# Performance work log

Measured on AMD Instinct MI355X. Metric: run time of the kernel, lower is better.

The kernel has to match this reference:

```python
import jax, jax.numpy as jnp
import numpy as np

SCALE_BASE = 512.0
GAMMA = 0.96875


def _rotate_every_two(x):
    x1 = x[..., ::2]
    x2 = x[..., 1::2]
    return jnp.stack([-x2, x1], axis=-1).reshape(x.shape)


def _dup_interleave(m):
    # [L, d/2] -> [L, d], each column duplicated: (a,b) -> (a,a,b,b)
    return jnp.repeat(m, 2, axis=-1)


def _xpos(x, downscale=False):
    # x: [B, L, d]; offset = 0 (parallel form)
    B, L, d = x.shape
    half = d // 2
    pos = jnp.arange(L, dtype=x.dtype)
    # xpos per-channel scale base
    sv = (jnp.arange(0, d, 2, dtype=x.dtype) + 0.4 * d) / (1.4 * d)   # [d/2]
    scale = sv[None, :] ** (pos[:, None] / SCALE_BASE)                 # [L, d/2]
    if downscale:
        scale = 1.0 / scale
    inv_freq = 1.0 / (10000.0 ** (jnp.arange(half, dtype=x.dtype) / half))
    sinusoid = pos[:, None] * inv_freq[None, :]                        # [L, d/2]
    sin = _dup_interleave(jnp.sin(sinusoid) * scale)                   # [L, d]
    cos = _dup_interleave(jnp.cos(sinusoid) * scale)                   # [L, d]
    return x * cos[None] + _rotate_every_two(x) * sin[None]


def _get_D(seq_len, dtype):
    idx = jnp.arange(seq_len)
    diff = idx[:, None] - idx[None, :]                                 # n - m
    safe = jnp.where(diff >= 0, diff, 0).astype(dtype)
    return jnp.where(diff >= 0, GAMMA ** safe, jnp.zeros((), dtype))   # [L, L]


def setup_inputs() -> dict:
    key = jax.random.key(0)
    k1, k2, k3, k4 = jax.random.split(key, 4)
    B, L, H, D = 2, 4096, 1024, 64
    X = jax.random.normal(k1, (B, L, H), dtype=jnp.float32)
    W_Q = jax.random.normal(k2, (H, D), dtype=jnp.float32) / H
    W_K = jax.random.normal(k3, (H, D), dtype=jnp.float32) / H
    W_V = jax.random.normal(k4, (H, D), dtype=jnp.float32) / H
    return {"X": X, "W_Q": W_Q, "W_K": W_K, "W_V": W_V}


def reference(X, W_Q, W_K, W_V):
    L = X.shape[1]
    Dmask = _get_D(L, X.dtype)                     # [L, L]
    Q = _xpos(X @ W_Q)                             # [B, L, d]
    K = _xpos(X @ W_K, downscale=True)             # [B, L, d]
    V = X @ W_V                                    # [B, L, v]
    ret = jnp.einsum('bnd,bmd->bnm', Q, K) * Dmask[None]  # [B, L, L]
    return ret @ V                                 # [B, L, v]
```

## Files before the change

### kernel.cpp

```cpp
#include <hip/hip_runtime.h>
#include <math.h>

#define NB 2
#define LL 4096
#define HH 1024
#define DD 64
#define CHK 64
#define NCH 64
#define BLROWS (NB*LL)
#define NCHT (NB*NCH)
#define GAMMA 0.96875f

typedef _Float16 f16x8 __attribute__((ext_vector_type(8)));
typedef _Float16 f16x4 __attribute__((ext_vector_type(4)));
typedef float    f32x4 __attribute__((ext_vector_type(4)));

#define WCH 12288
#define SBS 584

__global__ __launch_bounds__(256) void prep_w(
    const float* __restrict__ WQ, const float* __restrict__ WK,
    const float* __restrict__ WV, _Float16* __restrict__ Whg,
    _Float16* __restrict__ Wlg)
{
    const unsigned t = blockIdx.x * 256 + threadIdx.x;
    const unsigned kchunk = t / 1536u;
    const unsigned s = t - kchunk * 1536u;
    const int ct2  = s >> 6;
    const int lane = s & 63;
    const int n16  = ct2 >> 1;
    const int kt   = ct2 & 1;
    const int quad = lane >> 4;
    const int n    = n16 * 16 + (lane & 15);
    const int k0   = (int)kchunk * 64 + kt * 32 + quad * 8;
    const int m    = n >> 6;
    const int d    = n & 63;
    const float* Wm = (m == 0) ? WQ : (m == 1) ? WK : WV;
    f16x8 hv, lv;
#pragma unroll
    for (int j = 0; j < 8; ++j) {
        const float x = Wm[(size_t)(k0 + j) * DD + d] * 1024.f;
        const _Float16 h = (_Float16)x;
        hv[j] = h;
        lv[j] = (_Float16)(x - (float)h);
    }
    *(f16x8*)&Whg[(size_t)t * 8] = hv;
    *(f16x8*)&Wlg[(size_t)t * 8] = lv;
}

__global__ __launch_bounds__(256) void proj_mfma(
    const float* __restrict__ X, const _Float16* __restrict__ Whg,
    const _Float16* __restrict__ Wlg, _Float16* __restrict__ Qr,
    _Float16* __restrict__ Kf, _Float16* __restrict__ Vf)
{
    __shared__ __align__(16) _Float16 lds[12288];
    _Float16* Xh = lds;
    _Float16* Xl = lds + 2048;
    _Float16* Wh = lds + 4096;
    _Float16* Wl = lds + 8192;

    const int tid  = threadIdx.x;
    const int wv   = tid >> 6;
    const int lane = tid & 63;
    const int quad = lane >> 4;
    const int l15  = lane & 15;
    const int r0   = (blockIdx.x & 255) * 32;
    const int cb4  = (blockIdx.x >> 8) * 4;
    const int rt   = wv & 1;
    const int cp   = (wv >> 1) * 2;

    const int xrow = tid >> 3;
    const int xk8  = (tid & 7) * 8;
    const int xslot = (((xrow >> 4) * 2 + (xk8 >> 5)) * 64 +
                       ((xk8 >> 3) & 3) * 16 + (xrow & 15)) * 8;

    f32x4 acc[2];
    acc[0] = (f32x4){0.f, 0.f, 0.f, 0.f};
    acc[1] = (f32x4){0.f, 0.f, 0.f, 0.f};

    float4 pxa, pxb;
    f16x8  pwh[2], pwl2[2];
    {
        const float* xp = &X[(size_t)(r0 + xrow) * HH + xk8];
        pxa = *(const float4*)&xp[0];
        pxb = *(const float4*)&xp[4];
#pragma unroll
        for (int i = 0; i < 2; ++i) {
            const int s = tid + i * 256;
            const int ctl = s >> 7, kt = (s >> 6) & 1, ln = s & 63;
            const size_t off = (size_t)(((cb4 + ctl) * 2 + kt) * 64 + ln) * 8;
            pwh[i]  = *(const f16x8*)&Whg[off];
            pwl2[i] = *(const f16x8*)&Wlg[off];
        }
    }

    for (int ch = 0; ch < 16; ++ch) {
        __syncthreads();
        {
            const float xv[8] = {pxa.x, pxa.y, pxa.z, pxa.w,
                                 pxb.x, pxb.y, pxb.z, pxb.w};
            f16x8 hv, lv;
#pragma unroll
            for (int e = 0; e < 8; ++e) {
                const _Float16 h = (_Float16)xv[e];
                hv[e] = h;
                lv[e] = (_Float16)(xv[e] - (float)h);
            }
            *(f16x8*)&Xh[xslot] = hv;
            *(f16x8*)&Xl[xslot] = lv;
#pragma unroll
            for (int i = 0; i < 2; ++i) {
                *(f16x8*)&Wh[(tid + i * 256) * 8] = pwh[i];
                *(f16x8*)&Wl[(tid + i * 256) * 8] = pwl2[i];
            }
        }
        __syncthreads();
        if (ch + 1 < 16) {
            const float* xp = &X[(size_t)(r0 + xrow) * HH + (ch + 1) * 64 + xk8];
            pxa = *(const float4*)&xp[0];
            pxb = *(const float4*)&xp[4];
            const size_t cb = (size_t)(ch + 1) * WCH;
#pragma unroll
            for (int i = 0; i < 2; ++i) {
                const int s = tid + i * 256;
                const int ctl = s >> 7, kt = (s >> 6) & 1, ln = s & 63;
                const size_t off = cb +
                    (size_t)(((cb4 + ctl) * 2 + kt) * 64 + ln) * 8;
                pwh[i]  = *(const f16x8*)&Whg[off];
                pwl2[i] = *(const f16x8*)&Wlg[off];
            }
        }
#pragma unroll
        for (int kt = 0; kt < 2; ++kt) {
            const f16x8 aH = *(const f16x8*)&Xh[((rt * 2 + kt) * 64 + lane) * 8];
            const f16x8 aL = *(const f16x8*)&Xl[((rt * 2 + kt) * 64 + lane) * 8];
#pragma unroll
            for (int cj = 0; cj < 2; ++cj) {
                const int ctl = cp + cj;
                const f16x8 bh = *(const f16x8*)&Wh[((ctl * 2 + kt) * 64 + lane) * 8];
                const f16x8 bl = *(const f16x8*)&Wl[((ctl * 2 + kt) * 64 + lane) * 8];
                acc[cj] = __builtin_amdgcn_mfma_f32_16x16x32_f16(aH, bh, acc[cj], 0, 0, 0);
                acc[cj] = __builtin_amdgcn_mfma_f32_16x16x32_f16(aH, bl, acc[cj], 0, 0, 0);
                acc[cj] = __builtin_amdgcn_mfma_f32_16x16x32_f16(aL, bh, acc[cj], 0, 0, 0);
            }
        }
    }

#pragma unroll
    for (int cj = 0; cj < 2; ++cj) {
        const int ctg = cb4 + cp + cj;
        const f32x4 v = acc[cj];
        const int col = ctg * 16 + l15;
        const int mat = ctg >> 2;
        const int d   = col & 63;
        if (mat < 2) {
            const int i2 = d >> 1;
            const float sv   = (2.f * (float)i2 + 25.6f) / 89.6f;
            const float l2sv = log2f(sv);
            const float ifr  = exp2f(-13.28771237954945f * ((float)i2 / 32.f));
            const float sgn  = (mat == 0) ? 1.f : -1.f;
#pragma unroll
            for (int r = 0; r < 4; ++r) {
                const int row = r0 + rt * 16 + quad * 4 + r;
                const float val = v[r] * (1.f / 1024.f);
                const float p = __shfl_xor(val, 1, 64);
                const float pf  = (float)(row & (LL - 1));
                const float pfs = (float)(row & 63);
                const float scl = exp2f(sgn * (pfs * (1.f / 512.f)) * l2sv);
                float s, c;
                sincosf(pf * ifr, &s, &c);
                s *= scl; c *= scl;
                const float o = ((col & 1) == 0) ? val * c - p * s
                                                 : val * c + p * s;
                if (mat == 0) {
                    Qr[(size_t)row * DD + d] = (_Float16)o;
                } else {
                    const int b = row >> 12, posb = row & 4095;
                    Kf[(((size_t)b * 8 + (d >> 3)) * 4096 + posb) * 8 + (d & 7)] =
                        (_Float16)o;
                }
            }
        } else {
            f16x4 vv;
#pragma unroll
            for (int r = 0; r < 4; ++r) vv[r] = (_Float16)(v[r] * (1.f / 1024.f));
            const int row0 = r0 + rt * 16 + quad * 4;
            const int b = row0 >> 12, posb = row0 & 4095;
            *(f16x4*)&Vf[(((size_t)b * 512 + (posb >> 3)) * 64 + d) * 8 + (posb & 7)] = vv;
        }
    }
}

__global__ __launch_bounds__(256) void chunk_out(
    const _Float16* __restrict__ Qr, const _Float16* __restrict__ Kf,
    const _Float16* __restrict__ Vf, float* __restrict__ out)
{
    __shared__ __align__(16) unsigned char smraw[20032];
    _Float16* Sb  = (_Float16*)smraw;
    _Float16* svp = (_Float16*)(smraw + 18688);
    float*    pwl = (float*)(smraw + 19712);

    const int tid   = threadIdx.x;
    const int bc    = blockIdx.x;
    const int chunk = bc >> 2;
    const int qt    = bc & 3;
    const int w     = tid >> 6;
    const int lane  = tid & 63;
    const int quad  = lane >> 4;
    const int l15   = lane & 15;
    const int cloc  = chunk & 63;
    const int bB    = chunk >> 6;
    const size_t rowbase = (size_t)chunk * CHK + qt * 16;
    const float l2g = log2f(GAMMA);

    if (tid < 65) pwl[tid] = exp2f((float)tid * l2g);
#pragma unroll
    for (int e = 0; e < 2; ++e) {
        const int idx = tid + e * 256;
        const int dl  = (idx >> 6) + 1;
        const int dd  = idx & 63;
        const float sv = (2.f * (float)(dd >> 1) + 25.6f) / 89.6f;
        svp[idx] = (_Float16)exp2f(0.125f * (float)dl * log2f(sv));
    }

    f16x8 aQ[2];
#pragma unroll
    for (int ks = 0; ks < 2; ++ks)
        aQ[ks] = *(const f16x8*)&Qr[(rowbase + l15) * DD + ks * 32 + quad * 8];
    __syncthreads();

    {
        const int posb = cloc * 64 + w * 16 + l15;
        f32x4 sA = (f32x4){0.f, 0.f, 0.f, 0.f};
#pragma unroll
        for (int ks = 0; ks < 2; ++ks) {
            const f16x8 bK = *(const f16x8*)&Kf[(((size_t)bB * 8 + ks * 4 + quad)
                                                * 4096 + posb) * 8];
            sA = __builtin_amdgcn_mfma_f32_16x16x32_f16(aQ[ks], bK, sA, 0, 0, 0);
        }
        const int m = w * 16 + l15;
#pragma unroll
        for (int r = 0; r < 4; ++r) {
            const int nl = quad * 4 + r;
            const int n64 = qt * 16 + nl;
            const float val = (n64 >= m) ? sA[r] * pwl[n64 - m] : 0.f;
            Sb[nl * SBS + m] = (_Float16)val;
        }
    }

    for (int jc = w; jc < 32; jc += 4) {
        const int dlt = 8 - (jc >> 2);
        const bool valid = (dlt <= cloc);
        const int mq = (jc * 16 + l15) & 63;
        const float gl = valid ? exp2f((float)(64 * dlt - mq) * l2g) : 0.f;
        const _Float16 glh = (_Float16)gl;
        const int cs = valid ? (chunk - dlt) : chunk;
        const int posb = (cs & 63) * 64 + mq;
        f32x4 sc4 = (f32x4){0.f, 0.f, 0.f, 0.f};
#pragma unroll
        for (int ks = 0; ks < 2; ++ks) {
            const f16x8 bk = *(const f16x8*)&Kf[(((size_t)bB * 8 + ks * 4 + quad)
                                                * 4096 + posb) * 8];
            const f16x8 sv8 = *(const f16x8*)&svp[(dlt - 1) * 64 + ks * 32 + quad * 8];
            f16x8 b2;
#pragma unroll
            for (int j = 0; j < 8; ++j) b2[j] = bk[j] * glh * sv8[j];
            sc4 = __builtin_amdgcn_mfma_f32_16x16x32_f16(aQ[ks], b2, sc4, 0, 0, 0);
        }
#pragma unroll
        for (int r = 0; r < 4; ++r) {
            const int nl = quad * 4 + r;
            const int na = qt * 16 + nl;
            Sb[nl * SBS + 64 + jc * 16 + l15] = (_Float16)(sc4[r] * pwl[na]);
        }
    }
    __syncthreads();

    f32x4 oA = (f32x4){0.f, 0.f, 0.f, 0.f};
    const int dp = w * 16 + l15;
    for (int ks5 = 0; ks5 < 18; ++ks5) {
        const f16x8 aS = *(const f16x8*)&Sb[l15 * SBS + ks5 * 32 + quad * 8];
        const int m0 = ks5 * 32 + quad * 8;
        int gr;
        if (ks5 < 2) {
            gr = chunk * 64 + m0;
        } else {
            const int mc = m0 - 64;
            int cs2 = chunk - 8 + (mc >> 6);
            if (cs2 < (chunk & ~63)) cs2 = chunk;
            gr = cs2 * 64 + (mc & 63);
        }
        const int b2 = gr >> 12, pb = gr & 4095;
        const size_t vb = ((size_t)b2 * 512 + (pb >> 3)) * 64;
        const f16x8 bV = *(const f16x8*)&Vf[(vb + dp) * 8];
        oA = __builtin_amdgcn_mfma_f32_16x16x32_f16(aS, bV, oA, 0, 0, 0);
    }
#pragma unroll
    for (int r = 0; r < 4; ++r)
        out[(rowbase + quad * 4 + r) * DD + dp] = oA[r];
}

extern "C" void kernel_launch(void* const* d_in, const int* in_sizes, int n_in,
                              void* d_out, int out_size, void* d_ws, size_t ws_size,
                              hipStream_t stream)
{
    const float* X  = (const float*)d_in[0];
    const float* WQ = (const float*)d_in[1];
    const float* WK = (const float*)d_in[2];
    const float* WV = (const float*)d_in[3];
    float* outp = (float*)d_out;

    _Float16* Whg = (_Float16*)d_ws;
    _Float16* Wlg = Whg + 196608;
    _Float16* Qr  = Wlg + 196608;
    _Float16* Kf  = Qr + (size_t)BLROWS * DD;
    _Float16* Vf  = Kf + (size_t)BLROWS * DD;

    hipLaunchKernelGGL(prep_w, dim3(96), dim3(256), 0, stream,
                       WQ, WK, WV, Whg, Wlg);
    hipLaunchKernelGGL(proj_mfma, dim3(768), dim3(256), 0, stream,
                       X, Whg, Wlg, Qr, Kf, Vf);
    hipLaunchKernelGGL(chunk_out, dim3(512), dim3(256), 0, stream,
                       Qr, Kf, Vf, outp);
}
```

Baseline: 109.6 us.

## Drop split-fp16 error compensation and restructure projection without LDS

```diff
diff --git a/kernel.cpp b/kernel.cpp
--- a/kernel.cpp
+++ b/kernel.cpp
@@ -20,8 +20,7 @@
 
 __global__ __launch_bounds__(256) void prep_w(
     const float* __restrict__ WQ, const float* __restrict__ WK,
-    const float* __restrict__ WV, _Float16* __restrict__ Whg,
-    _Float16* __restrict__ Wlg)
+    const float* __restrict__ WV, _Float16* __restrict__ Wf)
 {
     const unsigned t = blockIdx.x * 256 + threadIdx.x;
     const unsigned kchunk = t / 1536u;
@@ -36,119 +35,85 @@
     const int m    = n >> 6;
     const int d    = n & 63;
     const float* Wm = (m == 0) ? WQ : (m == 1) ? WK : WV;
-    f16x8 hv, lv;
-#pragma unroll
-    for (int j = 0; j < 8; ++j) {
-        const float x = Wm[(size_t)(k0 + j) * DD + d] * 1024.f;
-        const _Float16 h = (_Float16)x;
-        hv[j] = h;
-        lv[j] = (_Float16)(x - (float)h);
-    }
-    *(f16x8*)&Whg[(size_t)t * 8] = hv;
-    *(f16x8*)&Wlg[(size_t)t * 8] = lv;
+    f16x8 hv;
+#pragma unroll
+    for (int j = 0; j < 8; ++j)
+        hv[j] = (_Float16)(Wm[(size_t)(k0 + j) * DD + d] * 1024.f);
+    *(f16x8*)&Wf[(size_t)t * 8] = hv;
 }
 
 __global__ __launch_bounds__(256) void proj_mfma(
-    const float* __restrict__ X, const _Float16* __restrict__ Whg,
-    const _Float16* __restrict__ Wlg, _Float16* __restrict__ Qr,
-    _Float16* __restrict__ Kf, _Float16* __restrict__ Vf)
-{
-    __shared__ __align__(16) _Float16 lds[12288];
-    _Float16* Xh = lds;
-    _Float16* Xl = lds + 2048;
-    _Float16* Wh = lds + 4096;
-    _Float16* Wl = lds + 8192;
-
+    const float* __restrict__ X, const _Float16* __restrict__ Wf,
+    _Float16* __restrict__ Qr, _Float16* __restrict__ Kf,
+    _Float16* __restrict__ Vf)
+{
     const int tid  = threadIdx.x;
     const int wv   = tid >> 6;
     const int lane = tid & 63;
     const int quad = lane >> 4;
     const int l15  = lane & 15;
-    const int r0   = (blockIdx.x & 255) * 32;
-    const int cb4  = (blockIdx.x >> 8) * 4;
-    const int rt   = wv & 1;
-    const int cp   = (wv >> 1) * 2;
-
-    const int xrow = tid >> 3;
-    const int xk8  = (tid & 7) * 8;
-    const int xslot = (((xrow >> 4) * 2 + (xk8 >> 5)) * 64 +
-                       ((xk8 >> 3) & 3) * 16 + (xrow & 15)) * 8;
-
-    f32x4 acc[2];
-    acc[0] = (f32x4){0.f, 0.f, 0.f, 0.f};
-    acc[1] = (f32x4){0.f, 0.f, 0.f, 0.f};
-
-    float4 pxa, pxb;
-    f16x8  pwh[2], pwl2[2];
+    const int rg   = blockIdx.x;
+    const size_t xrow = (size_t)(rg * 16 + l15) * HH;
+
+    f32x4 acc[3];
+#pragma unroll
+    for (int i = 0; i < 3; ++i) acc[i] = (f32x4){0.f, 0.f, 0.f, 0.f};
+
+    float4 pA[4];
+    f16x8  pB[6];
     {
-        const float* xp = &X[(size_t)(r0 + xrow) * HH + xk8];
-        pxa = *(const float4*)&xp[0];
-        pxb = *(const float4*)&xp[4];
-#pragma unroll
-        for (int i = 0; i < 2; ++i) {
-            const int s = tid + i * 256;
-            const int ctl = s >> 7, kt = (s >> 6) & 1, ln = s & 63;
-            const size_t off = (size_t)(((cb4 + ctl) * 2 + kt) * 64 + ln) * 8;
-            pwh[i]  = *(const f16x8*)&Whg[off];
-            pwl2[i] = *(const f16x8*)&Wlg[off];
-        }
+        const float* xp = &X[xrow + quad * 8];
+        pA[0] = *(const float4*)&xp[0];
+        pA[1] = *(const float4*)&xp[4];
+        pA[2] = *(const float4*)&xp[32];
+        pA[3] = *(const float4*)&xp[36];
+#pragma unroll
+        for (int cj = 0; cj < 3; ++cj)
+#pragma unroll
+            for (int kt = 0; kt < 2; ++kt)
+                pB[cj * 2 + kt] = *(const f16x8*)&Wf[
+                    (size_t)((((wv * 3 + cj) * 2 + kt) * 64 + lane)) * 8];
     }
 
     for (int ch = 0; ch < 16; ++ch) {
-        __syncthreads();
-        {
-            const float xv[8] = {pxa.x, pxa.y, pxa.z, pxa.w,
-                                 pxb.x, pxb.y, pxb.z, pxb.w};
-            f16x8 hv, lv;
-#pragma unroll
-            for (int e = 0; e < 8; ++e) {
-                const _Float16 h = (_Float16)xv[e];
-                hv[e] = h;
-                lv[e] = (_Float16)(xv[e] - (float)h);
-            }
-            *(f16x8*)&Xh[xslot] = hv;
-            *(f16x8*)&Xl[xslot] = lv;
-#pragma unroll
-            for (int i = 0; i < 2; ++i) {
-                *(f16x8*)&Wh[(tid + i * 256) * 8] = pwh[i];
-                *(f16x8*)&Wl[(tid + i * 256) * 8] = pwl2[i];
-            }
-        }
-        __syncthreads();
+        f16x8 a[2];
+#pragma unroll
+        for (int kt = 0; kt < 2; ++kt) {
+            const float4 xa = pA[kt * 2], xb = pA[kt * 2 + 1];
+            a[kt][0] = (_Float16)xa.x; a[kt][1] = (_Float16)xa.y;
+            a[kt][2] = (_Float16)xa.z; a[kt][3] = (_Float16)xa.w;
+            a[kt][4] = (_Float16)xb.x; a[kt][5] = (_Float16)xb.y;
+            a[kt][6] = (_Float16)xb.z; a[kt][7] = (_Float16)xb.w;
+        }
+        f16x8 b[6];
+#pragma unroll
+        for (int i = 0; i < 6; ++i) b[i] = pB[i];
+
         if (ch + 1 < 16) {
-            const float* xp = &X[(size_t)(r0 + xrow) * HH + (ch + 1) * 64 + xk8];
-            pxa = *(const float4*)&xp[0];
-            pxb = *(const float4*)&xp[4];
+            const float* xp = &X[xrow + (ch + 1) * 64 + quad * 8];
+            pA[0] = *(const float4*)&xp[0];
+            pA[1] = *(const float4*)&xp[4];
+            pA[2] = *(const float4*)&xp[32];
+            pA[3] = *(const float4*)&xp[36];
             const size_t cb = (size_t)(ch + 1) * WCH;
 #pragma unroll
-            for (int i = 0; i < 2; ++i) {
-                const int s = tid + i * 256;
-                const int ctl = s >> 7, kt = (s >> 6) & 1, ln = s & 63;
-                const size_t off = cb +
-                    (size_t)(((cb4 + ctl) * 2 + kt) * 64 + ln) * 8;
-                pwh[i]  = *(const f16x8*)&Whg[off];
-                pwl2[i] = *(const f16x8*)&Wlg[off];
-            }
-        }
-#pragma unroll
-        for (int kt = 0; kt < 2; ++kt) {
-            const f16x8 aH = *(const f16x8*)&Xh[((rt * 2 + kt) * 64 + lane) * 8];
-            const f16x8 aL = *(const f16x8*)&Xl[((rt * 2 + kt) * 64 + lane) * 8];
-#pragma unroll
-            for (int cj = 0; cj < 2; ++cj) {
-                const int ctl = cp + cj;
-                const f16x8 bh = *(const f16x8*)&Wh[((ctl * 2 + kt) * 64 + lane) * 8];
-                const f16x8 bl = *(const f16x8*)&Wl[((ctl * 2 + kt) * 64 + lane) * 8];
-                acc[cj] = __builtin_amdgcn_mfma_f32_16x16x32_f16(aH, bh, acc[cj], 0, 0, 0);
-                acc[cj] = __builtin_amdgcn_mfma_f32_16x16x32_f16(aH, bl, acc[cj], 0, 0, 0);
-                acc[cj] = __builtin_amdgcn_mfma_f32_16x16x32_f16(aL, bh, acc[cj], 0, 0, 0);
-            }
-        }
-    }
-
-#pragma unroll
-    for (int cj = 0; cj < 2; ++cj) {
-        const int ctg = cb4 + cp + cj;
+            for (int cj = 0; cj < 3; ++cj)
+#pragma unroll
+                for (int kt = 0; kt < 2; ++kt)
+                    pB[cj * 2 + kt] = *(const f16x8*)&Wf[cb +
+                        (size_t)((((wv * 3 + cj) * 2 + kt) * 64 + lane)) * 8];
+        }
+#pragma unroll
+        for (int kt = 0; kt < 2; ++kt)
+#pragma unroll
+            for (int cj = 0; cj < 3; ++cj)
+                acc[cj] = __builtin_amdgcn_mfma_f32_16x16x32_f16(
+                    a[kt], b[cj * 2 + kt], acc[cj], 0, 0, 0);
+    }
+
+#pragma unroll
+    for (int cj = 0; cj < 3; ++cj) {
+        const int ctg = wv * 3 + cj;
         const f32x4 v = acc[cj];
         const int col = ctg * 16 + l15;
         const int mat = ctg >> 2;
@@ -161,7 +126,7 @@
             const float sgn  = (mat == 0) ? 1.f : -1.f;
 #pragma unroll
             for (int r = 0; r < 4; ++r) {
-                const int row = r0 + rt * 16 + quad * 4 + r;
+                const int row = rg * 16 + quad * 4 + r;
                 const float val = v[r] * (1.f / 1024.f);
                 const float p = __shfl_xor(val, 1, 64);
                 const float pf  = (float)(row & (LL - 1));
@@ -175,8 +140,8 @@
                 if (mat == 0) {
                     Qr[(size_t)row * DD + d] = (_Float16)o;
                 } else {
-                    const int b = row >> 12, posb = row & 4095;
-                    Kf[(((size_t)b * 8 + (d >> 3)) * 4096 + posb) * 8 + (d & 7)] =
+                    const int b2 = row >> 12, posb = row & 4095;
+                    Kf[(((size_t)b2 * 8 + (d >> 3)) * 4096 + posb) * 8 + (d & 7)] =
                         (_Float16)o;
                 }
             }
@@ -184,9 +149,9 @@
             f16x4 vv;
 #pragma unroll
             for (int r = 0; r < 4; ++r) vv[r] = (_Float16)(v[r] * (1.f / 1024.f));
-            const int row0 = r0 + rt * 16 + quad * 4;
-            const int b = row0 >> 12, posb = row0 & 4095;
-            *(f16x4*)&Vf[(((size_t)b * 512 + (posb >> 3)) * 64 + d) * 8 + (posb & 7)] = vv;
+            const int row0 = rg * 16 + quad * 4;
+            const int b2 = row0 >> 12, posb = row0 & 4095;
+            *(f16x4*)&Vf[(((size_t)b2 * 512 + (posb >> 3)) * 64 + d) * 8 + (posb & 7)] = vv;
         }
     }
 }
@@ -310,16 +275,15 @@
     const float* WV = (const float*)d_in[3];
     float* outp = (float*)d_out;
 
-    _Float16* Whg = (_Float16*)d_ws;
-    _Float16* Wlg = Whg + 196608;
-    _Float16* Qr  = Wlg + 196608;
-    _Float16* Kf  = Qr + (size_t)BLROWS * DD;
-    _Float16* Vf  = Kf + (size_t)BLROWS * DD;
+    _Float16* Wf = (_Float16*)d_ws;
+    _Float16* Qr = Wf + 196608;
+    _Float16* Kf = Qr + (size_t)BLROWS * DD;
+    _Float16* Vf = Kf + (size_t)BLROWS * DD;
 
     hipLaunchKernelGGL(prep_w, dim3(96), dim3(256), 0, stream,
-                       WQ, WK, WV, Whg, Wlg);
-    hipLaunchKernelGGL(proj_mfma, dim3(768), dim3(256), 0, stream,
-                       X, Whg, Wlg, Qr, Kf, Vf);
+                       WQ, WK, WV, Wf);
+    hipLaunchKernelGGL(proj_mfma, dim3(512), dim3(256), 0, stream,
+                       X, Wf, Qr, Kf, Vf);
     hipLaunchKernelGGL(chunk_out, dim3(512), dim3(256), 0, stream,
                        Qr, Kf, Vf, outp);
 }
```

After: 106.7 us. 2.7% less time.
